# Kernel optimization log

Measured on AMD Instinct MI355X. Metric: run time of the kernel, lower is better.

## Reference

```python
import jax, jax.numpy as jnp
import numpy as np

N_TASK = 50000
N_EDGE = 50000
E = 500000
F_TASK = 64
F_EDGE = 64
H = 256
OUT = 256


def _lin(key, fan_in, fan_out):
    kw, kb = jax.random.split(key)
    lim = 1.0 / np.sqrt(fan_in)
    W = jax.random.uniform(kw, (fan_in, fan_out), minval=-lim, maxval=lim, dtype=jnp.float32)
    b = jax.random.uniform(kb, (fan_out,), minval=-lim, maxval=lim, dtype=jnp.float32)
    return W, b


def setup_inputs() -> dict:
    key = jax.random.key(0)
    ks = jax.random.split(key, 20)
    inp = {}
    inp['task_features'] = jax.random.normal(ks[0], (N_TASK, F_TASK), dtype=jnp.float32)
    inp['edge_features'] = jax.random.normal(ks[1], (N_EDGE, F_EDGE), dtype=jnp.float32)
    inp['queue_edges'] = jax.random.randint(ks[2], (2, E), 0, N_TASK)
    inp['type_edges'] = jax.random.randint(ks[3], (2, E), 0, N_TASK)
    inp['affinity_edges'] = jax.random.randint(ks[4], (2, E), 0, N_TASK)  # src<num_tasks, tgt<num_edges
    inp['topology_edges'] = jax.random.randint(ks[5], (2, E), 0, N_EDGE)
    inp['te_w1'], inp['te_b1'] = _lin(ks[6], F_TASK, H)
    inp['te_w2'], inp['te_b2'] = _lin(ks[7], H, H)
    inp['ee_w1'], inp['ee_b1'] = _lin(ks[8], F_EDGE, H)
    inp['ee_w2'], inp['ee_b2'] = _lin(ks[9], H, H)
    inp['gnn_w0'], inp['gnn_b0'] = _lin(ks[10], H, H)
    inp['gnn_w1'], inp['gnn_b1'] = _lin(ks[11], H, H)
    inp['ta_w'], inp['ta_b'] = _lin(ks[12], H, H)
    inp['ea_w'], inp['ea_b'] = _lin(ks[13], H, H)
    inp['out_w1'], inp['out_b1'] = _lin(ks[14], 2 * H, H)
    inp['out_w2'], inp['out_b2'] = _lin(ks[15], H, OUT)
    return inp


def _mean_msg(src_emb, src, tgt, num_segments):
    # scatter-add messages from src nodes into tgt slots, divide by in-degree (clamped >=1)
    msgs = jax.ops.segment_sum(src_emb[src], tgt, num_segments=num_segments)
    cnt = jax.ops.segment_sum(jnp.ones_like(src, dtype=src_emb.dtype), tgt, num_segments=num_segments)
    return msgs / jnp.maximum(cnt, 1.0)[:, None]


def _forward(task_features, edge_features, queue_edges, type_edges, affinity_edges, topology_edges,
             te_w1, te_b1, te_w2, te_b2, ee_w1, ee_b1, ee_w2, ee_b2,
             gnn_w0, gnn_b0, gnn_w1, gnn_b1, ta_w, ta_b, ea_w, ea_b,
             out_w1, out_b1, out_w2, out_b2):
    relu = jax.nn.relu
    # node encoders (Linear-ReLU-Linear-ReLU)
    t = relu(relu(task_features @ te_w1 + te_b1) @ te_w2 + te_b2)   # [N_task, H]
    e = relu(relu(edge_features @ ee_w1 + ee_b1) @ ee_w2 + ee_b2)   # [N_edge, H]

    # queue convolution: messages computed ONCE from original t (torch code never updates task_embeddings in loop)
    qs, qt = queue_edges[0], queue_edges[1]
    q_msgs = jax.ops.segment_sum(t[qs], qt, num_segments=t.shape[0])
    h = t
    for W, b in ((gnn_w0, gnn_b0), (gnn_w1, gnn_b1)):
        h = relu((h + 0.5 * q_msgs) @ W + b)
    t = h

    # type convolution: mean-aggregated same-type messages
    t = t + 0.3 * _mean_msg(t, type_edges[0], type_edges[1], t.shape[0])

    # affinity convolution: bipartite task<->edge exchange (simultaneous update)
    asrc, atgt = affinity_edges[0], affinity_edges[1]
    t_msgs = jax.ops.segment_sum(e[atgt], asrc, num_segments=t.shape[0])
    t_cnt = jax.ops.segment_sum(jnp.ones((asrc.shape[0],), t.dtype), asrc, num_segments=t.shape[0])
    e_msgs = jax.ops.segment_sum(t[asrc], atgt, num_segments=e.shape[0])
    e_cnt = jax.ops.segment_sum(jnp.ones((atgt.shape[0],), e.dtype), atgt, num_segments=e.shape[0])
    t_new = t + 0.3 * t_msgs / jnp.maximum(t_cnt, 1.0)[:, None]
    e_new = e + 0.3 * e_msgs / jnp.maximum(e_cnt, 1.0)[:, None]
    t, e = t_new, e_new

    # topology convolution: edge-edge mean aggregation
    e = e + 0.3 * _mean_msg(e, topology_edges[0], topology_edges[1], e.shape[0])

    # graph-level aggregation
    t_agg = relu(jnp.mean(t, axis=0) @ ta_w + ta_b)  # [H]
    e_agg = relu(jnp.mean(e, axis=0) @ ea_w + ea_b)  # [H]
    combined = jnp.concatenate([t_agg, e_agg], axis=0)  # [2H]
    out = relu(combined @ out_w1 + out_b1) @ out_w2 + out_b2  # [OUT]
    return out


def reference(task_features, edge_features, queue_edges, type_edges, affinity_edges, topology_edges,
              te_w1, te_b1, te_w2, te_b2, ee_w1, ee_b1, ee_w2, ee_b2,
              gnn_w0, gnn_b0, gnn_w1, gnn_b1, ta_w, ta_b, ea_w, ea_b,
              out_w1, out_b1, out_w2, out_b2):
    return _forward(task_features, edge_features, queue_edges, type_edges, affinity_edges, topology_edges,
                    te_w1, te_b1, te_w2, te_b2, ee_w1, ee_b1, ee_w2, ee_b2,
                    gnn_w0, gnn_b0, gnn_w1, gnn_b1, ta_w, ta_b, ea_w, ea_b,
                    out_w1, out_b1, out_w2, out_b2)
```

## Files before the change

### kernel.cpp

```cpp
#include <hip/hip_runtime.h>

#define H 256
#define NT 50000
#define NEDGE 50000
#define NE 500000

#define NBKT 391
#define NBLK 123
#define CHUNK 4096
#define CAP 2816

typedef __attribute__((ext_vector_type(8))) short short8_t;
typedef __attribute__((ext_vector_type(4))) float f32x4;
typedef unsigned short u16;
typedef unsigned int u32;

__device__ __forceinline__ void fatomic(float* p, float v) { unsafeAtomicAdd(p, v); }

__device__ __forceinline__ float b2f(u16 v) { return __uint_as_float((u32)v << 16); }
__device__ __forceinline__ u16 f2b(float f) {
    u32 u = __float_as_uint(f);
    u += 0x7FFFu + ((u >> 16) & 1u);
    return (u16)(u >> 16);
}

__device__ __forceinline__ u32 f2fp8_1(float f) {
    u32 u = __float_as_uint(f);
    u32 s = (u >> 24) & 0x80u;
    float af = fabsf(f);
    if (af >= 448.f) return s | 0x7Eu;
    if (af < 0.015625f) {
        int m = (int)rintf(af * 512.0f);
        return s | (u32)m;
    }
    u32 au = __float_as_uint(af);
    u32 r = au + 0x7FFFFu + ((au >> 20) & 1u);
    int e = (int)(r >> 23) - 127;
    return s | (u32)(((e + 7) << 3) | ((r >> 20) & 7u));
}
__device__ __forceinline__ float fp82f_1(u32 b) {
    u32 s = (b & 0x80u) << 24;
    u32 em = b & 0x7Fu;
    float v;
    if (em >= 8) v = __uint_as_float((((em >> 3) + 120u) << 23) | ((em & 7u) << 20));
    else v = (float)em * 0.001953125f;
    return __uint_as_float(__float_as_uint(v) | s);
}
__device__ __forceinline__ u32 pk4_fp8(float a, float b, float c, float d) {
#if __has_builtin(__builtin_amdgcn_cvt_pk_fp8_f32)
    u32 r = 0;
    r = (u32)__builtin_amdgcn_cvt_pk_fp8_f32(a, b, (int)r, false);
    r = (u32)__builtin_amdgcn_cvt_pk_fp8_f32(c, d, (int)r, true);
    return r;
#else
    return f2fp8_1(a) | (f2fp8_1(b) << 8) | (f2fp8_1(c) << 16) | (f2fp8_1(d) << 24);
#endif
}
__device__ __forceinline__ float4 unpk4_fp8(u32 v) {
#if __has_builtin(__builtin_amdgcn_cvt_pk_f32_fp8)
    auto lo = __builtin_amdgcn_cvt_pk_f32_fp8(v, false);
    auto hi = __builtin_amdgcn_cvt_pk_f32_fp8(v, true);
    return make_float4(lo[0], lo[1], hi[0], hi[1]);
#else
    return make_float4(fp82f_1(v & 255u), fp82f_1((v >> 8) & 255u),
                       fp82f_1((v >> 16) & 255u), fp82f_1(v >> 24));
#endif
}

__device__ __forceinline__ const int* pick_list(
    int l, const int* a, const int* b, const int* c, const int* d, const int* e)
{ return (l == 0) ? a : (l == 1) ? b : (l == 2) ? c : (l == 3) ? d : e; }

template<int K1, bool FUSE_Q, bool XF32, bool DUAL>
__global__ __launch_bounds__(256) void fused_mlp(
    const void* __restrict__ XA, const u16* __restrict__ Q,
    const u16* __restrict__ W1hA, const u16* __restrict__ W1lA, const float* __restrict__ b1A,
    const u16* __restrict__ W2hA, const u16* __restrict__ W2lA, const float* __restrict__ b2A,
    u16* __restrict__ outA, u32* __restrict__ f8A,
    const void* __restrict__ XB,
    const u16* __restrict__ W1hB, const u16* __restrict__ W1lB, const float* __restrict__ b1B,
    const u16* __restrict__ W2hB, const u16* __restrict__ W2lB, const float* __restrict__ b2B,
    u16* __restrict__ outB, u32* __restrict__ f8B,
    int N, int nA, float s2)
{
    __shared__ u16 lds[64 * 256];
    int bid = blockIdx.x;
    const void* X = XA;
    const u16 *W1h = W1hA, *W1l = W1lA, *W2h = W2hA, *W2l = W2lA;
    const float *b1 = b1A, *b2 = b2A;
    u16* out = outA;
    u32* f8 = f8A;
    if (DUAL && bid >= nA) {
        bid -= nA; X = XB;
        W1h = W1hB; W1l = W1lB; b1 = b1B;
        W2h = W2hB; W2l = W2lB; b2 = b2B;
        out = outB; f8 = f8B;
    }
    const int m0 = bid * 64;

    constexpr int RCH = K1 / 8;
    for (int i = threadIdx.x; i < 64 * RCH; i += 256) {
        int r = i / RCH, c8 = i % RCH;
        int gr = m0 + r; if (gr >= N) gr = N - 1;
        uint4 v;
        if (XF32) {
            const float* xf = (const float*)X + (size_t)gr * K1 + c8 * 8;
            float4 a = *(const float4*)xf;
            float4 b = *(const float4*)(xf + 4);
            v.x = (u32)f2b(a.x) | ((u32)f2b(a.y) << 16);
            v.y = (u32)f2b(a.z) | ((u32)f2b(a.w) << 16);
            v.z = (u32)f2b(b.x) | ((u32)f2b(b.y) << 16);
            v.w = (u32)f2b(b.z) | ((u32)f2b(b.w) << 16);
        } else {
            v = *(const uint4*)((const u16*)X + (size_t)gr * K1 + c8 * 8);
        }
        u32 byte = (u32)(r * (K1 * 2) + c8 * 16) ^ (u32)((r & 7) << 4);
        *(uint4*)((char*)lds + byte) = v;
    }
    __syncthreads();

    const int wv = threadIdx.x >> 6, l = threadIdx.x & 63;
    const int li = l & 15, lk = l >> 4;

    f32x4 acc[4][4];
    #pragma unroll
    for (int i = 0; i < 4; i++)
        #pragma unroll
        for (int j = 0; j < 4; j++)
            acc[i][j] = (f32x4){0.f, 0.f, 0.f, 0.f};

    #pragma unroll
    for (int k0 = 0; k0 < K1; k0 += 32) {
        short8_t xb[4];
        #pragma unroll
        for (int mi = 0; mi < 4; mi++) {
            int m = mi * 16 + li;
            u32 byte = (u32)(m * (K1 * 2) + (k0 + lk * 8) * 2) ^ (u32)((m & 7) << 4);
            xb[mi] = *(const short8_t*)((const char*)lds + byte);
        }
        #pragma unroll
        for (int ni = 0; ni < 4; ni++) {
            const size_t wi = (size_t)((wv * 4 + ni) * (K1 / 32) + (k0 >> 5)) * 64 + l;
            short8_t wh = ((const short8_t*)W1h)[wi];
            short8_t wl = ((const short8_t*)W1l)[wi];
            #pragma unroll
            for (int mi = 0; mi < 4; mi++) {
                acc[mi][ni] = __builtin_amdgcn_mfma_f32_16x16x32_bf16(wl, xb[mi], acc[mi][ni], 0, 0, 0);
                acc[mi][ni] = __builtin_amdgcn_mfma_f32_16x16x32_bf16(wh, xb[mi], acc[mi][ni], 0, 0, 0);
            }
        }
    }

    __syncthreads();

    #pragma unroll
    for (int ni = 0; ni < 4; ni++) {
        int c = wv * 64 + ni * 16 + lk * 4;
        float4 b4 = *(const float4*)(b1 + c);
        #pragma unroll
        for (int mi = 0; mi < 4; mi++) {
            int m = mi * 16 + li;
            float o0 = fmaxf(acc[mi][ni][0] + b4.x, 0.f);
            float o1 = fmaxf(acc[mi][ni][1] + b4.y, 0.f);
            float o2 = fmaxf(acc[mi][ni][2] + b4.z, 0.f);
            float o3 = fmaxf(acc[mi][ni][3] + b4.w, 0.f);
            if (FUSE_Q) {
                int gm = m0 + m; if (gm >= N) gm = N - 1;
                uint2 qv = *(const uint2*)(Q + (size_t)gm * 256 + c);
                o0 = fmaf(s2, b2f((u16)(qv.x & 0xFFFF)), o0);
                o1 = fmaf(s2, b2f((u16)(qv.x >> 16)), o1);
                o2 = fmaf(s2, b2f((u16)(qv.y & 0xFFFF)), o2);
                o3 = fmaf(s2, b2f((u16)(qv.y >> 16)), o3);
            }
            u32 w0 = (u32)f2b(o0) | ((u32)f2b(o1) << 16);
            u32 w1 = (u32)f2b(o2) | ((u32)f2b(o3) << 16);
            u32 byte = (u32)(m * 512 + c * 2) ^ (u32)((m & 7) << 4);
            *(uint2*)((char*)lds + byte) = make_uint2(w0, w1);
        }
    }
    __syncthreads();

    #pragma unroll
    for (int i = 0; i < 4; i++)
        #pragma unroll
        for (int j = 0; j < 4; j++)
            acc[i][j] = (f32x4){0.f, 0.f, 0.f, 0.f};

    #pragma unroll
    for (int k0 = 0; k0 < 256; k0 += 32) {
        short8_t xb[4];
        #pragma unroll
        for (int mi = 0; mi < 4; mi++) {
            int m = mi * 16 + li;
            u32 byte = (u32)(m * 512 + (k0 + lk * 8) * 2) ^ (u32)((m & 7) << 4);
            xb[mi] = *(const short8_t*)((const char*)lds + byte);
        }
        #pragma unroll
        for (int ni = 0; ni < 4; ni++) {
            const size_t wi = (size_t)((wv * 4 + ni) * 8 + (k0 >> 5)) * 64 + l;
            short8_t wh = ((const short8_t*)W2h)[wi];
            short8_t wl = ((const short8_t*)W2l)[wi];
            #pragma unroll
            for (int mi = 0; mi < 4; mi++) {
                acc[mi][ni] = __builtin_amdgcn_mfma_f32_16x16x32_bf16(wl, xb[mi], acc[mi][ni], 0, 0, 0);
                acc[mi][ni] = __builtin_amdgcn_mfma_f32_16x16x32_bf16(wh, xb[mi], acc[mi][ni], 0, 0, 0);
            }
        }
    }

    #pragma unroll
    for (int mi = 0; mi < 4; mi++) {
        int m = m0 + mi * 16 + li;
        if (m < N) {
            #pragma unroll
            for (int ni = 0; ni < 4; ni++) {
                int c = wv * 64 + ni * 16 + lk * 4;
                float4 b4 = *(const float4*)(b2 + c);
                float o0 = fmaxf(acc[mi][ni][0] + b4.x, 0.f);
                float o1 = fmaxf(acc[mi][ni][1] + b4.y, 0.f);
                float o2 = fmaxf(acc[mi][ni][2] + b4.z, 0.f);
                float o3 = fmaxf(acc[mi][ni][3] + b4.w, 0.f);
                u32 w0 = (u32)f2b(o0) | ((u32)f2b(o1) << 16);
                u32 w1 = (u32)f2b(o2) | ((u32)f2b(o3) << 16);
                *(uint2*)(out + (size_t)m * H + c) = make_uint2(w0, w1);
                if (f8) f8[(size_t)m * 64 + (c >> 2)] = pk4_fp8(o0, o1, o2, o3);
            }
        }
    }
}

__global__ __launch_bounds__(256) void wt_pack(
    const float* __restrict__ s0, const float* __restrict__ s1,
    const float* __restrict__ s2, const float* __restrict__ s3,
    const float* __restrict__ s4, const float* __restrict__ s5,
    u16* __restrict__ arena)
{
    const int li = blockIdx.y;
    const int K = (li == 0 || li == 4) ? 64 : 256;
    const int offs[6] = {0, 32768, 163840, 294912, 425984, 458752};
    int n = K * 256;
    int i = blockIdx.x * 256 + threadIdx.x;
    if (i >= n) return;
    const float* W = (li == 0) ? s0 : (li == 1) ? s1 : (li == 2) ? s2
                   : (li == 3) ? s3 : (li == 4) ? s4 : s5;
    u16* hi = arena + offs[li];
    u16* lo = hi + n;
    int k = i >> 8, c = i & 255;
    float u = W[i];
    u32 b = __float_as_uint(u);
    float r = u - __uint_as_float(b & 0xFFFF0000u);
    int lane = ((k >> 3) & 3) * 16 + (c & 15);
    size_t idx = ((size_t)((c >> 4) * (K >> 5) + (k >> 5)) * 64 + lane) * 8 + (k & 7);
    hi[idx] = (u16)(b >> 16);
    lo[idx] = f2b(r);
}

__global__ __launch_bounds__(256) void hist_kernel(
    const int* __restrict__ k0, const int* __restrict__ k1, const int* __restrict__ k2,
    const int* __restrict__ k3, const int* __restrict__ k4, int* __restrict__ counts)
{
    __shared__ int h[NBKT];
    int l = blockIdx.y;
    const int* k = pick_list(l, k0, k1, k2, k3, k4);
    for (int i = threadIdx.x; i < NBKT; i += 256) h[i] = 0;
    __syncthreads();
    int e0 = blockIdx.x * CHUNK;
    for (int i = threadIdx.x; i < CHUNK; i += 256) {
        int e = e0 + i;
        if (e < NE) atomicAdd(&h[k[e] >> 7], 1);
    }
    __syncthreads();
    int* out = counts + ((size_t)l * NBLK + blockIdx.x) * NBKT;
    for (int i = threadIdx.x; i < NBKT; i += 256) out[i] = h[i];
}

__global__ __launch_bounds__(256) void scan_buckets(
    const int* __restrict__ counts, int* __restrict__ starts, int* __restrict__ bases)
{
    __shared__ int buf[256];
    int l = blockIdx.x, t = threadIdx.x;
    const int* cl = counts + (size_t)l * NBLK * NBKT;
    int* sl = starts + (size_t)l * NBLK * NBKT;
    int b0 = t * 2;
    int totloc[2];
    int s = 0;
    #pragma unroll
    for (int j = 0; j < 2; j++) {
        int b = b0 + j, v = 0;
        if (b < NBKT) for (int k = 0; k < NBLK; k++) v += cl[k * NBKT + b];
        totloc[j] = v; s += v;
    }
    buf[t] = s; __syncthreads();
    for (int st = 1; st < 256; st <<= 1) {
        int v = (t >= st) ? buf[t - st] : 0; __syncthreads();
        buf[t] += v; __syncthreads();
    }
    int run = buf[t] - s;
    #pragma unroll
    for (int j = 0; j < 2; j++) {
        int b = b0 + j;
        if (b < NBKT) {
            bases[l * (NBKT + 1) + b] = run;
            int p = run;
            for (int k = 0; k < NBLK; k++) { sl[k * NBKT + b] = p; p += cl[k * NBKT + b]; }
            run += totloc[j];
        }
    }
    if (t == 255) bases[l * (NBKT + 1) + NBKT] = NE;
}

__global__ __launch_bounds__(256) void partition_kernel(
    const int* __restrict__ k0, const int* __restrict__ k1, const int* __restrict__ k2,
    const int* __restrict__ k3, const int* __restrict__ k4,
    const int* __restrict__ v0, const int* __restrict__ v1, const int* __restrict__ v2,
    const int* __restrict__ v3, const int* __restrict__ v4,
    const int* __restrict__ starts, int* __restrict__ csr)
{
    __shared__ u32 ent[CHUNK];
    __shared__ u16 ebk[CHUNK];
    __shared__ int cnt[NBKT], loff[NBKT], cur[NBKT], gst[NBKT];
    __shared__ int buf[256];
    int l = blockIdx.y, t = threadIdx.x;
    const int* k = pick_list(l, k0, k1, k2, k3, k4);
    const int* v = pick_list(l, v0, v1, v2, v3, v4);
    const int* st = starts + ((size_t)l * NBLK + blockIdx.x) * NBKT;
    for (int i = t; i < NBKT; i += 256) { cnt[i] = 0; gst[i] = st[i]; }
    __syncthreads();
    int e0 = blockIdx.x * CHUNK;
    u32 ep[16]; int eb[16];
    #pragma unroll
    for (int j = 0; j < 16; j++) {
        int e = e0 + j * 256 + t;
        if (e < NE) {
            int key = k[e];
            eb[j] = key >> 7;
            ep[j] = ((u32)(key & 127) << 16) | (u32)v[e];
            atomicAdd(&cnt[eb[j]], 1);
        } else eb[j] = -1;
    }
    __syncthreads();
    int b0 = t * 2;
    int c0 = (b0 < NBKT) ? cnt[b0] : 0;
    int c1 = (b0 + 1 < NBKT) ? cnt[b0 + 1] : 0;
    int s = c0 + c1;
    buf[t] = s; __syncthreads();
    for (int stp = 1; stp < 256; stp <<= 1) {
        int x = (t >= stp) ? buf[t - stp] : 0; __syncthreads();
        buf[t] += x; __syncthreads();
    }
    int run = buf[t] - s;
    if (b0 < NBKT)     { loff[b0] = run;          cur[b0] = run; }
    if (b0 + 1 < NBKT) { loff[b0 + 1] = run + c0; cur[b0 + 1] = run + c0; }
    __syncthreads();
    #pragma unroll
    for (int j = 0; j < 16; j++) {
        if (eb[j] >= 0) {
            int p = atomicAdd(&cur[eb[j]], 1);
            ent[p] = ep[j]; ebk[p] = (u16)eb[j];
        }
    }
    __syncthreads();
    int nv = min(CHUNK, NE - e0);
    int* c = csr + (size_t)l * NE;
    for (int i = t; i < nv; i += 256) {
        int b = ebk[i];
        c[gst[b] + (i - loff[b])] = (int)ent[i];
    }
}

__global__ __launch_bounds__(256) void bucket_csr(
    const int* __restrict__ bases, int* __restrict__ csr, int* __restrict__ off)
{
    __shared__ int seg[CAP];
    __shared__ int hist[128], scn[128];
    int l = blockIdx.y, b = blockIdx.x, t = threadIdx.x;
    int base = bases[l * (NBKT + 1) + b];
    int end  = bases[l * (NBKT + 1) + b + 1];
    int sz = end - base; if (sz > CAP) sz = CAP;
    int* c = csr + (size_t)l * NE;
    for (int i = t; i < sz; i += 256) seg[i] = c[base + i];
    if (t < 128) hist[t] = 0;
    __syncthreads();
    for (int i = t; i < sz; i += 256) atomicAdd(&hist[seg[i] >> 16], 1);
    __syncthreads();
    if (t < 128) scn[t] = hist[t];
    __syncthreads();
    for (int st = 1; st < 128; st <<= 1) {
        int v = 0;
        if (t < 128 && t >= st) v = scn[t - st];
        __syncthreads();
        if (t < 128) scn[t] += v;
        __syncthreads();
    }
    if (t < 128) {
        int key = b * 128 + t;
        int excl = scn[t] - hist[t];
        if (key < NT) off[l * (NT + 1) + key] = base + excl;
        hist[t] = excl;
    }
    if (b == 0 && t == 128) off[l * (NT + 1) + NT] = NE;
    __syncthreads();
    for (int i = t; i < sz; i += 256) {
        int u = seg[i];
        int p = atomicAdd(&hist[u >> 16], 1);
        c[base + p] = u & 0xFFFF;
    }
}

__global__ __launch_bounds__(256) void gather_q(
    const u16* __restrict__ src, const int* __restrict__ csr,
    const int* __restrict__ off, u16* __restrict__ sumOut,
    u16* __restrict__ fuseOut, float s2, int N)
{
    int r = (blockIdx.x * 256 + threadIdx.x) >> 6;
    int lane = threadIdx.x & 63;
    if (r >= N) return;
    int o0 = off[r];
    int d  = off[r + 1] - o0;
    const ushort4* s4 = (const ushort4*)src;
    float4 acc = {0.f, 0.f, 0.f, 0.f};
    int j = 0;
    for (; j + 4 <= d; j += 4) {
        int i0 = csr[o0 + j], i1 = csr[o0 + j + 1];
        int i2 = csr[o0 + j + 2], i3 = csr[o0 + j + 3];
        ushort4 a = s4[(size_t)i0 * 64 + lane];
        ushort4 b = s4[(size_t)i1 * 64 + lane];
        ushort4 c = s4[(size_t)i2 * 64 + lane];
        ushort4 e = s4[(size_t)i3 * 64 + lane];
        acc.x += b2f(a.x) + b2f(b.x) + b2f(c.x) + b2f(e.x);
        acc.y += b2f(a.y) + b2f(b.y) + b2f(c.y) + b2f(e.y);
        acc.z += b2f(a.z) + b2f(b.z) + b2f(c.z) + b2f(e.z);
        acc.w += b2f(a.w) + b2f(b.w) + b2f(c.w) + b2f(e.w);
    }
    for (; j < d; j++) {
        ushort4 v = s4[(size_t)csr[o0 + j] * 64 + lane];
        acc.x += b2f(v.x); acc.y += b2f(v.y);
        acc.z += b2f(v.z); acc.w += b2f(v.w);
    }
    ushort4 pk;
    pk.x = f2b(acc.x); pk.y = f2b(acc.y); pk.z = f2b(acc.z); pk.w = f2b(acc.w);
    ((ushort4*)(sumOut + (size_t)r * H))[lane] = pk;
    ushort4 b = s4[(size_t)r * 64 + lane];
    pk.x = f2b(fmaf(s2, acc.x, b2f(b.x)));
    pk.y = f2b(fmaf(s2, acc.y, b2f(b.y)));
    pk.z = f2b(fmaf(s2, acc.z, b2f(b.z)));
    pk.w = f2b(fmaf(s2, acc.w, b2f(b.w)));
    ((ushort4*)(fuseOut + (size_t)r * H))[lane] = pk;
}

__global__ __launch_bounds__(256) void gather_mean_f8(
    const u32* __restrict__ srcA, const int* __restrict__ csrA, const int* __restrict__ offA,
    const u16* __restrict__ baseA, u16* __restrict__ dstA, u32* __restrict__ m8A,
    const u32* __restrict__ srcB, const int* __restrict__ csrB, const int* __restrict__ offB,
    const u16* __restrict__ baseB, u16* __restrict__ dstB, u32* __restrict__ m8B,
    float alpha, int nA, int N)
{
    int bid = blockIdx.x;
    const u32* src = srcA; const int* csr = csrA; const int* off = offA;
    const u16* base = baseA; u16* dst = dstA; u32* m8 = m8A;
    if (bid >= nA) {
        bid -= nA; src = srcB; csr = csrB; off = offB; base = baseB; dst = dstB; m8 = m8B;
    }
    int r = (bid * 256 + threadIdx.x) >> 6;
    int lane = threadIdx.x & 63;
    if (r >= N) return;
    int o0 = off[r];
    int d  = off[r + 1] - o0;
    float4 acc = {0.f, 0.f, 0.f, 0.f};
    int j = 0;
    for (; j + 4 <= d; j += 4) {
        u32 a = src[(size_t)csr[o0 + j]     * 64 + lane];
        u32 b = src[(size_t)csr[o0 + j + 1] * 64 + lane];
        u32 c = src[(size_t)csr[o0 + j + 2] * 64 + lane];
        u32 e = src[(size_t)csr[o0 + j + 3] * 64 + lane];
        float4 fa = unpk4_fp8(a), fb = unpk4_fp8(b), fc = unpk4_fp8(c), fe = unpk4_fp8(e);
        acc.x += fa.x + fb.x + fc.x + fe.x;
        acc.y += fa.y + fb.y + fc.y + fe.y;
        acc.z += fa.z + fb.z + fc.z + fe.z;
        acc.w += fa.w + fb.w + fc.w + fe.w;
    }
    for (; j < d; j++) {
        float4 f = unpk4_fp8(src[(size_t)csr[o0 + j] * 64 + lane]);
        acc.x += f.x; acc.y += f.y; acc.z += f.z; acc.w += f.w;
    }
    float s = alpha / (float)max(d, 1);
    ushort4 b = ((const ushort4*)(base + (size_t)r * H))[lane];
    float o0f = fmaf(s, acc.x, b2f(b.x));
    float o1f = fmaf(s, acc.y, b2f(b.y));
    float o2f = fmaf(s, acc.z, b2f(b.z));
    float o3f = fmaf(s, acc.w, b2f(b.w));
    ushort4 pk;
    pk.x = f2b(o0f); pk.y = f2b(o1f); pk.z = f2b(o2f); pk.w = f2b(o3f);
    ((ushort4*)(dst + (size_t)r * H))[lane] = pk;
    if (m8) m8[(size_t)r * 64 + lane] = pk4_fp8(o0f, o1f, o2f, o3f);
}

__global__ __launch_bounds__(256) void colsum2(
    const u16* __restrict__ embA, float* __restrict__ accA,
    const u16* __restrict__ embB, float* __restrict__ accB, int N)
{
    const u16* emb = embA; float* acc = accA;
    int blk = blockIdx.x;
    if (blk >= 256) { blk -= 256; emb = embB; acc = accB; }
    int c = threadIdx.x;
    float s = 0.f;
    for (int r = blk; r < N; r += 256)
        s += b2f(emb[(size_t)r * H + c]);
    fatomic(&acc[c], s);
}

__global__ __launch_bounds__(256) void final_mlp(
    const float* __restrict__ sumT, const float* __restrict__ sumE,
    float invNT, float invNE,
    const float* __restrict__ ta_w, const float* __restrict__ ta_b,
    const float* __restrict__ ea_w, const float* __restrict__ ea_b,
    const float* __restrict__ ow1, const float* __restrict__ ob1,
    const float* __restrict__ ow2, const float* __restrict__ ob2,
    float* __restrict__ out)
{
    __shared__ float tm[H], em[H], comb[2 * H], hid[H];
    int t = threadIdx.x;
    tm[t] = sumT[t] * invNT;
    em[t] = sumE[t] * invNE;
    __syncthreads();
    float s = ta_b[t];
    for (int k = 0; k < H; k++) s += tm[k] * ta_w[k * H + t];
    comb[t] = fmaxf(s, 0.f);
    s = ea_b[t];
    for (int k = 0; k < H; k++) s += em[k] * ea_w[k * H + t];
    comb[H + t] = fmaxf(s, 0.f);
    __syncthreads();
    s = ob1[t];
    for (int k = 0; k < 2 * H; k++) s += comb[k] * ow1[k * H + t];
    hid[t] = fmaxf(s, 0.f);
    __syncthreads();
    s = ob2[t];
    for (int k = 0; k < H; k++) s += hid[k] * ow2[k * H + t];
    out[t] = s;
}

extern "C" void kernel_launch(void* const* d_in, const int* in_sizes, int n_in,
                              void* d_out, int out_size, void* d_ws, size_t ws_size,
                              hipStream_t stream) {
    const float* tf  = (const float*)d_in[0];
    const float* ef  = (const float*)d_in[1];
    const int*   qe  = (const int*)d_in[2];
    const int*   te  = (const int*)d_in[3];
    const int*   ae  = (const int*)d_in[4];
    const int*   pe  = (const int*)d_in[5];
    const float* te_w1 = (const float*)d_in[6];  const float* te_b1 = (const float*)d_in[7];
    const float* te_w2 = (const float*)d_in[8];  const float* te_b2 = (const float*)d_in[9];
    const float* ee_w1 = (const float*)d_in[10]; const float* ee_b1 = (const float*)d_in[11];
    const float* ee_w2 = (const float*)d_in[12]; const float* ee_b2 = (const float*)d_in[13];
    const float* gw0 = (const float*)d_in[14];   const float* gb0 = (const float*)d_in[15];
    const float* gw1 = (const float*)d_in[16];   const float* gb1 = (const float*)d_in[17];
    const float* ta_w = (const float*)d_in[18];  const float* ta_b = (const float*)d_in[19];
    const float* ea_w = (const float*)d_in[20];  const float* ea_b = (const float*)d_in[21];
    const float* ow1 = (const float*)d_in[22];   const float* ob1 = (const float*)d_in[23];
    const float* ow2 = (const float*)d_in[24];   const float* ob2 = (const float*)d_in[25];

    const size_t NB = (size_t)NT * H;
    u16* T  = (u16*)d_ws;
    u16* Bf = T + NB;
    u16* S  = Bf + NB;
    u16* F  = S + NB;
    float* sumT = (float*)(F + NB);
    float* sumE = sumT + H;
    int* off5   = (int*)(sumE + H);
    int* csr5   = off5 + 5 * (NT + 1);
    int* counts = csr5 + (size_t)5 * NE;
    int* starts = counts + (size_t)5 * NBLK * NBKT;
    int* bases  = starts + (size_t)5 * NBLK * NBKT;
    u16* arena = (u16*)(((size_t)counts + 15) & ~(size_t)15);
    u16* wt_te1_h = arena + 0;      u16* wt_te1_l = arena + 16384;
    u16* wt_te2_h = arena + 32768;  u16* wt_te2_l = arena + 98304;
    u16* wt_g0_h  = arena + 163840; u16* wt_g0_l  = arena + 229376;
    u16* wt_g1_h  = arena + 294912; u16* wt_g1_l  = arena + 360448;
    u16* wt_ee1_h = arena + 425984; u16* wt_ee1_l = arena + 442368;
    u16* wt_ee2_h = arena + 458752; u16* wt_ee2_l = arena + 524288;
    u32* M1 = (u32*)(((size_t)(bases + 5 * (NBKT + 1)) + 15) & ~(size_t)15);
    u32* M2 = M1 + NB / 4;
    u32* M3 = M2 + NB / 4;
    u32* M4 = M3 + NB / 4;

    const int MG = (NT + 63) / 64;
    const int GB = (NT * 64) / 256;

    const int *k0 = qe + NE, *k1 = te + NE, *k2 = ae,      *k3 = ae + NE, *k4 = pe + NE;
    const int *v0 = qe,      *v1 = te,      *v2 = ae + NE, *v3 = ae,      *v4 = pe;

    dim3 pg(NBLK, 5);
    hist_kernel<<<pg, 256, 0, stream>>>(k0, k1, k2, k3, k4, counts);
    scan_buckets<<<5, 256, 0, stream>>>(counts, starts, bases);
    partition_kernel<<<pg, 256, 0, stream>>>(k0, k1, k2, k3, k4, v0, v1, v2, v3, v4,
                                             starts, csr5);
    wt_pack<<<dim3(256, 6), 256, 0, stream>>>(te_w1, te_w2, gw0, gw1, ee_w1, ee_w2, arena);
    bucket_csr<<<dim3(NBKT, 5), 256, 0, stream>>>(bases, csr5, off5);

    #define LOFF(l) (off5 + (l) * (NT + 1))
    #define LCSR(l) (csr5 + (size_t)(l) * NE)

    fused_mlp<64, false, true, true><<<2 * MG, 256, 0, stream>>>(
        tf, nullptr, wt_te1_h, wt_te1_l, te_b1, wt_te2_h, wt_te2_l, te_b2, T, nullptr,
        ef, wt_ee1_h, wt_ee1_l, ee_b1, wt_ee2_h, wt_ee2_l, ee_b2, Bf, M2,
        NT, MG, 0.f);

    gather_q<<<GB, 256, 0, stream>>>(T, LCSR(0), LOFF(0), S, F, 0.5f, NT);

    fused_mlp<256, true, false, false><<<MG, 256, 0, stream>>>(
        F, S, wt_g0_h, wt_g0_l, gb0, wt_g1_h, wt_g1_l, gb1, T, M1,
        nullptr, nullptr, nullptr, nullptr, nullptr, nullptr, nullptr, nullptr, nullptr,
        NT, MG, 0.5f);

    gather_mean_f8<<<GB, 256, 0, stream>>>(
        M1, LCSR(1), LOFF(1), T, F, M3,
        M1, LCSR(1), LOFF(1), T, F, M3,
        0.3f, GB, NT);

    gather_mean_f8<<<2 * GB, 256, 0, stream>>>(
        M2, LCSR(2), LOFF(2), F, S, nullptr,
        M3, LCSR(3), LOFF(3), Bf, T, M4,
        0.3f, GB, NT);

    gather_mean_f8<<<GB, 256, 0, stream>>>(
        M4, LCSR(4), LOFF(4), T, Bf, nullptr,
        M4, LCSR(4), LOFF(4), T, Bf, nullptr,
        0.3f, GB, NT);

    hipMemsetAsync(sumT, 0, H * 4, stream);
    hipMemsetAsync(sumE, 0, H * 4, stream);
    colsum2<<<512, 256, 0, stream>>>(S, sumT, Bf, sumE, NT);
    final_mlp<<<1, 256, 0, stream>>>(sumT, sumE, 1.f / NT, 1.f / NEDGE,
                                     ta_w, ta_b, ea_w, ea_b, ow1, ob1, ow2, ob2,
                                     (float*)d_out);
}
```

Baseline: 467.3 us.

## Prefetch MLP weights one k-step ahead and gather queue messages from FP8 copy

The two GEMM loops in fused_mlp now load the next k-slice of split-bf16 weights into registers while the current slice's MFMAs run, and raise wave priority around the MFMA block. The aim is to hide global weight-load latency behind the matrix math. The encoder also writes an FP8 copy of the task embeddings (M0), which the queue gather now reads. That halves the bytes per random neighbor read compared with bf16, at the cost of lower precision in the queue message sums and more live registers.

Result: faster. 430.0 us (-8.0%).

```diff
diff --git a/kernel.cpp b/kernel.cpp
--- a/kernel.cpp
+++ b/kernel.cpp
@@ -129,24 +129,45 @@
         for (int j = 0; j < 4; j++)
             acc[i][j] = (f32x4){0.f, 0.f, 0.f, 0.f};
 
-    #pragma unroll
-    for (int k0 = 0; k0 < K1; k0 += 32) {
-        short8_t xb[4];
-        #pragma unroll
-        for (int mi = 0; mi < 4; mi++) {
-            int m = mi * 16 + li;
-            u32 byte = (u32)(m * (K1 * 2) + (k0 + lk * 8) * 2) ^ (u32)((m & 7) << 4);
-            xb[mi] = *(const short8_t*)((const char*)lds + byte);
-        }
+    {
+        constexpr int KS = K1 / 32;
+        short8_t whc[4], wlc[4];
         #pragma unroll
         for (int ni = 0; ni < 4; ni++) {
-            const size_t wi = (size_t)((wv * 4 + ni) * (K1 / 32) + (k0 >> 5)) * 64 + l;
-            short8_t wh = ((const short8_t*)W1h)[wi];
-            short8_t wl = ((const short8_t*)W1l)[wi];
+            const size_t wi = (size_t)((wv * 4 + ni) * KS) * 64 + l;
+            whc[ni] = ((const short8_t*)W1h)[wi];
+            wlc[ni] = ((const short8_t*)W1l)[wi];
+        }
+        #pragma unroll
+        for (int ks = 0; ks < KS; ks++) {
+            short8_t whn[4], wln[4];
+            if (ks + 1 < KS) {
+                #pragma unroll
+                for (int ni = 0; ni < 4; ni++) {
+                    const size_t wi = (size_t)((wv * 4 + ni) * KS + ks + 1) * 64 + l;
+                    whn[ni] = ((const short8_t*)W1h)[wi];
+                    wln[ni] = ((const short8_t*)W1l)[wi];
+                }
+            }
+            short8_t xb[4];
             #pragma unroll
             for (int mi = 0; mi < 4; mi++) {
-                acc[mi][ni] = __builtin_amdgcn_mfma_f32_16x16x32_bf16(wl, xb[mi], acc[mi][ni], 0, 0, 0);
-                acc[mi][ni] = __builtin_amdgcn_mfma_f32_16x16x32_bf16(wh, xb[mi], acc[mi][ni], 0, 0, 0);
+                int m = mi * 16 + li;
+                u32 byte = (u32)(m * (K1 * 2) + (ks * 32 + lk * 8) * 2) ^ (u32)((m & 7) << 4);
+                xb[mi] = *(const short8_t*)((const char*)lds + byte);
+            }
+            __builtin_amdgcn_s_setprio(1);
+            #pragma unroll
+            for (int ni = 0; ni < 4; ni++)
+                #pragma unroll
+                for (int mi = 0; mi < 4; mi++) {
+                    acc[mi][ni] = __builtin_amdgcn_mfma_f32_16x16x32_bf16(wlc[ni], xb[mi], acc[mi][ni], 0, 0, 0);
+                    acc[mi][ni] = __builtin_amdgcn_mfma_f32_16x16x32_bf16(whc[ni], xb[mi], acc[mi][ni], 0, 0, 0);
+                }
+            __builtin_amdgcn_s_setprio(0);
+            if (ks + 1 < KS) {
+                #pragma unroll
+                for (int ni = 0; ni < 4; ni++) { whc[ni] = whn[ni]; wlc[ni] = wln[ni]; }
             }
         }
     }
@@ -186,24 +207,44 @@
         for (int j = 0; j < 4; j++)
             acc[i][j] = (f32x4){0.f, 0.f, 0.f, 0.f};
 
-    #pragma unroll
-    for (int k0 = 0; k0 < 256; k0 += 32) {
-        short8_t xb[4];
-        #pragma unroll
-        for (int mi = 0; mi < 4; mi++) {
-            int m = mi * 16 + li;
-            u32 byte = (u32)(m * 512 + (k0 + lk * 8) * 2) ^ (u32)((m & 7) << 4);
-            xb[mi] = *(const short8_t*)((const char*)lds + byte);
-        }
+    {
+        short8_t whc[4], wlc[4];
         #pragma unroll
         for (int ni = 0; ni < 4; ni++) {
-            const size_t wi = (size_t)((wv * 4 + ni) * 8 + (k0 >> 5)) * 64 + l;
-            short8_t wh = ((const short8_t*)W2h)[wi];
-            short8_t wl = ((const short8_t*)W2l)[wi];
+            const size_t wi = (size_t)((wv * 4 + ni) * 8) * 64 + l;
+            whc[ni] = ((const short8_t*)W2h)[wi];
+            wlc[ni] = ((const short8_t*)W2l)[wi];
+        }
+        #pragma unroll
+        for (int ks = 0; ks < 8; ks++) {
+            short8_t whn[4], wln[4];
+            if (ks + 1 < 8) {
+                #pragma unroll
+                for (int ni = 0; ni < 4; ni++) {
+                    const size_t wi = (size_t)((wv * 4 + ni) * 8 + ks + 1) * 64 + l;
+                    whn[ni] = ((const short8_t*)W2h)[wi];
+                    wln[ni] = ((const short8_t*)W2l)[wi];
+                }
+            }
+            short8_t xb[4];
             #pragma unroll
             for (int mi = 0; mi < 4; mi++) {
-                acc[mi][ni] = __builtin_amdgcn_mfma_f32_16x16x32_bf16(wl, xb[mi], acc[mi][ni], 0, 0, 0);
-                acc[mi][ni] = __builtin_amdgcn_mfma_f32_16x16x32_bf16(wh, xb[mi], acc[mi][ni], 0, 0, 0);
+                int m = mi * 16 + li;
+                u32 byte = (u32)(m * 512 + (ks * 32 + lk * 8) * 2) ^ (u32)((m & 7) << 4);
+                xb[mi] = *(const short8_t*)((const char*)lds + byte);
+            }
+            __builtin_amdgcn_s_setprio(1);
+            #pragma unroll
+            for (int ni = 0; ni < 4; ni++)
+                #pragma unroll
+                for (int mi = 0; mi < 4; mi++) {
+                    acc[mi][ni] = __builtin_amdgcn_mfma_f32_16x16x32_bf16(wlc[ni], xb[mi], acc[mi][ni], 0, 0, 0);
+                    acc[mi][ni] = __builtin_amdgcn_mfma_f32_16x16x32_bf16(whc[ni], xb[mi], acc[mi][ni], 0, 0, 0);
+                }
+            __builtin_amdgcn_s_setprio(0);
+            if (ks + 1 < 8) {
+                #pragma unroll
+                for (int ni = 0; ni < 4; ni++) { whc[ni] = whn[ni]; wlc[ni] = wln[ni]; }
             }
         }
     }
@@ -407,40 +448,37 @@
     }
 }
 
-__global__ __launch_bounds__(256) void gather_q(
-    const u16* __restrict__ src, const int* __restrict__ csr,
-    const int* __restrict__ off, u16* __restrict__ sumOut,
-    u16* __restrict__ fuseOut, float s2, int N)
+__global__ __launch_bounds__(256) void gather_q_f8(
+    const u32* __restrict__ src, const int* __restrict__ csr,
+    const int* __restrict__ off, const u16* __restrict__ baseT,
+    u16* __restrict__ sumOut, u16* __restrict__ fuseOut, float s2, int N)
 {
     int r = (blockIdx.x * 256 + threadIdx.x) >> 6;
     int lane = threadIdx.x & 63;
     if (r >= N) return;
     int o0 = off[r];
     int d  = off[r + 1] - o0;
-    const ushort4* s4 = (const ushort4*)src;
     float4 acc = {0.f, 0.f, 0.f, 0.f};
     int j = 0;
     for (; j + 4 <= d; j += 4) {
-        int i0 = csr[o0 + j], i1 = csr[o0 + j + 1];
-        int i2 = csr[o0 + j + 2], i3 = csr[o0 + j + 3];
-        ushort4 a = s4[(size_t)i0 * 64 + lane];
-        ushort4 b = s4[(size_t)i1 * 64 + lane];
-        ushort4 c = s4[(size_t)i2 * 64 + lane];
-        ushort4 e = s4[(size_t)i3 * 64 + lane];
-        acc.x += b2f(a.x) + b2f(b.x) + b2f(c.x) + b2f(e.x);
-        acc.y += b2f(a.y) + b2f(b.y) + b2f(c.y) + b2f(e.y);
-        acc.z += b2f(a.z) + b2f(b.z) + b2f(c.z) + b2f(e.z);
-        acc.w += b2f(a.w) + b2f(b.w) + b2f(c.w) + b2f(e.w);
+        u32 a = src[(size_t)csr[o0 + j]     * 64 + lane];
+        u32 b = src[(size_t)csr[o0 + j + 1] * 64 + lane];
+        u32 c = src[(size_t)csr[o0 + j + 2] * 64 + lane];
+        u32 e = src[(size_t)csr[o0 + j + 3] * 64 + lane];
+        float4 fa = unpk4_fp8(a), fb = unpk4_fp8(b), fc = unpk4_fp8(c), fe = unpk4_fp8(e);
+        acc.x += fa.x + fb.x + fc.x + fe.x;
+        acc.y += fa.y + fb.y + fc.y + fe.y;
+        acc.z += fa.z + fb.z + fc.z + fe.z;
+        acc.w += fa.w + fb.w + fc.w + fe.w;
     }
     for (; j < d; j++) {
-        ushort4 v = s4[(size_t)csr[o0 + j] * 64 + lane];
-        acc.x += b2f(v.x); acc.y += b2f(v.y);
-        acc.z += b2f(v.z); acc.w += b2f(v.w);
+        float4 f = unpk4_fp8(src[(size_t)csr[o0 + j] * 64 + lane]);
+        acc.x += f.x; acc.y += f.y; acc.z += f.z; acc.w += f.w;
     }
     ushort4 pk;
     pk.x = f2b(acc.x); pk.y = f2b(acc.y); pk.z = f2b(acc.z); pk.w = f2b(acc.w);
     ((ushort4*)(sumOut + (size_t)r * H))[lane] = pk;
-    ushort4 b = s4[(size_t)r * 64 + lane];
+    ushort4 b = ((const ushort4*)(baseT + (size_t)r * H))[lane];
     pk.x = f2b(fmaf(s2, acc.x, b2f(b.x)));
     pk.y = f2b(fmaf(s2, acc.y, b2f(b.y)));
     pk.z = f2b(fmaf(s2, acc.z, b2f(b.z)));
@@ -578,7 +616,8 @@
     u16* wt_g1_h  = arena + 294912; u16* wt_g1_l  = arena + 360448;
     u16* wt_ee1_h = arena + 425984; u16* wt_ee1_l = arena + 442368;
     u16* wt_ee2_h = arena + 458752; u16* wt_ee2_l = arena + 524288;
-    u32* M1 = (u32*)(((size_t)(bases + 5 * (NBKT + 1)) + 15) & ~(size_t)15);
+    u32* M0 = (u32*)(((size_t)(bases + 5 * (NBKT + 1)) + 15) & ~(size_t)15);
+    u32* M1 = M0 + NB / 4;
     u32* M2 = M1 + NB / 4;
     u32* M3 = M2 + NB / 4;
     u32* M4 = M3 + NB / 4;
@@ -601,11 +640,11 @@
     #define LCSR(l) (csr5 + (size_t)(l) * NE)
 
     fused_mlp<64, false, true, true><<<2 * MG, 256, 0, stream>>>(
-        tf, nullptr, wt_te1_h, wt_te1_l, te_b1, wt_te2_h, wt_te2_l, te_b2, T, nullptr,
+        tf, nullptr, wt_te1_h, wt_te1_l, te_b1, wt_te2_h, wt_te2_l, te_b2, T, M0,
         ef, wt_ee1_h, wt_ee1_l, ee_b1, wt_ee2_h, wt_ee2_l, ee_b2, Bf, M2,
         NT, MG, 0.f);
 
-    gather_q<<<GB, 256, 0, stream>>>(T, LCSR(0), LOFF(0), S, F, 0.5f, NT);
+    gather_q_f8<<<GB, 256, 0, stream>>>(M0, LCSR(0), LOFF(0), T, S, F, 0.5f, NT);
 
     fused_mlp<256, true, false, false><<<MG, 256, 0, stream>>>(
         F, S, wt_g0_h, wt_g0_l, gb0, wt_g1_h, wt_g1_l, gb1, T, M1,
```
